# Kernel tuning notes

Hardware: AMD Instinct MI355X
Metric: run time of the kernel (lower is better)

## Reference

```python
import jax, jax.numpy as jnp
import numpy as np


def _linear_params(key, fan_in, fan_out):
    # torch nn.Linear default init: U(-1/sqrt(fan_in), 1/sqrt(fan_in))
    kw, kb = jax.random.split(key)
    bound = 1.0 / np.sqrt(fan_in)
    W = jax.random.uniform(kw, (fan_out, fan_in), jnp.float32, -bound, bound)
    b = jax.random.uniform(kb, (fan_out,), jnp.float32, -bound, bound)
    return W, b


def setup_inputs() -> dict:
    key = jax.random.key(0)
    kx, k1, k7, k8, k9 = jax.random.split(key, 5)
    x = jax.random.normal(kx, (4194304, 6), dtype=jnp.float32)
    W1, b1 = _linear_params(k1, 6, 8)
    W7, b7 = _linear_params(k7, 8, 4)
    W8, b8 = _linear_params(k8, 4, 2)
    W9, b9 = _linear_params(k9, 2, 1)
    return {"x": x, "W1": W1, "b1": b1, "W7": W7, "b7": b7,
            "W8": W8, "b8": b8, "W9": W9, "b9": b9}


def reference(x, W1, b1, W7, b7, W8, b8, W9, b9):
    # forward only uses l1 -> relu -> l7 -> relu -> l8 -> relu -> l9 -> softplus
    z = jax.nn.relu(x @ W1.T + b1)      # [N, 8]
    z = jax.nn.relu(z @ W7.T + b7)      # [N, 4]
    z = jax.nn.relu(z @ W8.T + b8)      # [N, 2]
    z = z @ W9.T + b9                   # [N, 1]
    return jax.nn.softplus(z)
```

## Files before the change

### kernel.cpp

```cpp
#include <hip/hip_runtime.h>
#include <math.h>


__device__ __forceinline__ float softplus_fast(float z) {
    float e = __expf(-fabsf(z));
    return fmaxf(z, 0.0f) + __logf(1.0f + e);
}

__global__ __launch_bounds__(256) void encoder_mlp_kernel(
    const float* __restrict__ x,
    const float* __restrict__ W1, const float* __restrict__ b1,
    const float* __restrict__ W7, const float* __restrict__ b7,
    const float* __restrict__ W8, const float* __restrict__ b8,
    const float* __restrict__ W9, const float* __restrict__ b9,
    float* __restrict__ out, int n_rows)
{
    const int t = blockIdx.x * blockDim.x + threadIdx.x;
    const long long row0 = (long long)t * 4;
    if (row0 >= n_rows) return;

    float xr[4][6];
    bool full_quad = (row0 + 4 <= n_rows);

    if (full_quad) {
        const float4* xin = reinterpret_cast<const float4*>(x) + (size_t)t * 6;
        float4 v0 = xin[0], v1 = xin[1], v2 = xin[2],
               v3 = xin[3], v4 = xin[4], v5 = xin[5];
        xr[0][0] = v0.x; xr[0][1] = v0.y; xr[0][2] = v0.z; xr[0][3] = v0.w; xr[0][4] = v1.x; xr[0][5] = v1.y;
        xr[1][0] = v1.z; xr[1][1] = v1.w; xr[1][2] = v2.x; xr[1][3] = v2.y; xr[1][4] = v2.z; xr[1][5] = v2.w;
        xr[2][0] = v3.x; xr[2][1] = v3.y; xr[2][2] = v3.z; xr[2][3] = v3.w; xr[2][4] = v4.x; xr[2][5] = v4.y;
        xr[3][0] = v4.z; xr[3][1] = v4.w; xr[3][2] = v5.x; xr[3][3] = v5.y; xr[3][4] = v5.z; xr[3][5] = v5.w;
    } else {
        #pragma unroll
        for (int r = 0; r < 4; ++r) {
            long long row = row0 + r;
            #pragma unroll
            for (int k = 0; k < 6; ++k)
                xr[r][k] = (row < n_rows) ? x[row * 6 + k] : 0.0f;
        }
    }

    float res[4];
    #pragma unroll
    for (int r = 0; r < 4; ++r) {
        float h1[8];
        #pragma unroll
        for (int j = 0; j < 8; ++j) {
            float acc = b1[j];
            #pragma unroll
            for (int k = 0; k < 6; ++k) acc = fmaf(W1[j * 6 + k], xr[r][k], acc);
            h1[j] = fmaxf(acc, 0.0f);
        }
        float h7[4];
        #pragma unroll
        for (int j = 0; j < 4; ++j) {
            float acc = b7[j];
            #pragma unroll
            for (int k = 0; k < 8; ++k) acc = fmaf(W7[j * 8 + k], h1[k], acc);
            h7[j] = fmaxf(acc, 0.0f);
        }
        float h8[2];
        #pragma unroll
        for (int j = 0; j < 2; ++j) {
            float acc = b8[j];
            #pragma unroll
            for (int k = 0; k < 4; ++k) acc = fmaf(W8[j * 4 + k], h7[k], acc);
            h8[j] = fmaxf(acc, 0.0f);
        }
        float z = fmaf(W9[0], h8[0], fmaf(W9[1], h8[1], b9[0]));
        res[r] = softplus_fast(z);
    }

    if (full_quad) {
        float4 o;
        o.x = res[0]; o.y = res[1]; o.z = res[2]; o.w = res[3];
        reinterpret_cast<float4*>(out)[t] = o;
    } else {
        #pragma unroll
        for (int r = 0; r < 4; ++r) {
            long long row = row0 + r;
            if (row < n_rows) out[row] = res[r];
        }
    }
}

extern "C" void kernel_launch(void* const* d_in, const int* in_sizes, int n_in,
                              void* d_out, int out_size, void* d_ws, size_t ws_size,
                              hipStream_t stream) {
    const float* x  = (const float*)d_in[0];
    const float* W1 = (const float*)d_in[1];
    const float* b1 = (const float*)d_in[2];
    const float* W7 = (const float*)d_in[3];
    const float* b7 = (const float*)d_in[4];
    const float* W8 = (const float*)d_in[5];
    const float* b8 = (const float*)d_in[6];
    const float* W9 = (const float*)d_in[7];
    const float* b9 = (const float*)d_in[8];
    float* out = (float*)d_out;

    const int n_rows = in_sizes[0] / 6;
    const int n_threads = (n_rows + 3) / 4;
    const int block = 256;
    const int grid = (n_threads + block - 1) / block;

    encoder_mlp_kernel<<<grid, block, 0, stream>>>(
        x, W1, b1, W7, b7, W8, b8, W9, b9, out, n_rows);
}
```

Before: 24.68 us.

## Process four quads per thread with double-buffered software-pipelined loads

Each thread now handles four row-quads strided by the grid size, loading the next quad into a second register buffer while computing the current one. The aim is more memory-level parallelism and load latency hidden behind the MLP arithmetic, with a quarter as many threads. The tail handling for row counts not divisible by four was dropped: partial quads are read and written as full float4 vectors, which can go out of bounds when n_rows is not a multiple of 4. It also raises register pressure.

```diff
diff --git a/kernel.cpp b/kernel.cpp
--- a/kernel.cpp
+++ b/kernel.cpp
@@ -1,46 +1,36 @@
 #include <hip/hip_runtime.h>
 #include <math.h>
 
+
+typedef float v4f __attribute__((ext_vector_type(4)));
 
 __device__ __forceinline__ float softplus_fast(float z) {
     float e = __expf(-fabsf(z));
     return fmaxf(z, 0.0f) + __logf(1.0f + e);
 }
 
-__global__ __launch_bounds__(256) void encoder_mlp_kernel(
-    const float* __restrict__ x,
+__device__ __forceinline__ void load_quad(const v4f* __restrict__ xin,
+                                          size_t q, v4f b[6]) {
+    const v4f* p = xin + q * 6;
+    b[0] = p[0]; b[1] = p[1]; b[2] = p[2];
+    b[3] = p[3]; b[4] = p[4]; b[5] = p[5];
+}
+
+__device__ __forceinline__ v4f compute_quad(
+    const v4f b[6],
     const float* __restrict__ W1, const float* __restrict__ b1,
     const float* __restrict__ W7, const float* __restrict__ b7,
     const float* __restrict__ W8, const float* __restrict__ b8,
-    const float* __restrict__ W9, const float* __restrict__ b9,
-    float* __restrict__ out, int n_rows)
+    const float* __restrict__ W9, const float* __restrict__ b9)
 {
-    const int t = blockIdx.x * blockDim.x + threadIdx.x;
-    const long long row0 = (long long)t * 4;
-    if (row0 >= n_rows) return;
+    float xr[4][6];
+    xr[0][0]=b[0].x; xr[0][1]=b[0].y; xr[0][2]=b[0].z; xr[0][3]=b[0].w; xr[0][4]=b[1].x; xr[0][5]=b[1].y;
+    xr[1][0]=b[1].z; xr[1][1]=b[1].w; xr[1][2]=b[2].x; xr[1][3]=b[2].y; xr[1][4]=b[2].z; xr[1][5]=b[2].w;
+    xr[2][0]=b[3].x; xr[2][1]=b[3].y; xr[2][2]=b[3].z; xr[2][3]=b[3].w; xr[2][4]=b[4].x; xr[2][5]=b[4].y;
+    xr[3][0]=b[4].z; xr[3][1]=b[4].w; xr[3][2]=b[5].x; xr[3][3]=b[5].y; xr[3][4]=b[5].z; xr[3][5]=b[5].w;
 
-    float xr[4][6];
-    bool full_quad = (row0 + 4 <= n_rows);
-
-    if (full_quad) {
-        const float4* xin = reinterpret_cast<const float4*>(x) + (size_t)t * 6;
-        float4 v0 = xin[0], v1 = xin[1], v2 = xin[2],
-               v3 = xin[3], v4 = xin[4], v5 = xin[5];
-        xr[0][0] = v0.x; xr[0][1] = v0.y; xr[0][2] = v0.z; xr[0][3] = v0.w; xr[0][4] = v1.x; xr[0][5] = v1.y;
-        xr[1][0] = v1.z; xr[1][1] = v1.w; xr[1][2] = v2.x; xr[1][3] = v2.y; xr[1][4] = v2.z; xr[1][5] = v2.w;
-        xr[2][0] = v3.x; xr[2][1] = v3.y; xr[2][2] = v3.z; xr[2][3] = v3.w; xr[2][4] = v4.x; xr[2][5] = v4.y;
-        xr[3][0] = v4.z; xr[3][1] = v4.w; xr[3][2] = v5.x; xr[3][3] = v5.y; xr[3][4] = v5.z; xr[3][5] = v5.w;
-    } else {
-        #pragma unroll
-        for (int r = 0; r < 4; ++r) {
-            long long row = row0 + r;
-            #pragma unroll
-            for (int k = 0; k < 6; ++k)
-                xr[r][k] = (row < n_rows) ? x[row * 6 + k] : 0.0f;
-        }
-    }
-
-    float res[4];
+    v4f res;
+    float out4[4];
     #pragma unroll
     for (int r = 0; r < 4; ++r) {
         float h1[8];
@@ -68,20 +58,48 @@
             h8[j] = fmaxf(acc, 0.0f);
         }
         float z = fmaf(W9[0], h8[0], fmaf(W9[1], h8[1], b9[0]));
-        res[r] = softplus_fast(z);
+        out4[r] = softplus_fast(z);
     }
+    res.x = out4[0]; res.y = out4[1]; res.z = out4[2]; res.w = out4[3];
+    return res;
+}
 
-    if (full_quad) {
-        float4 o;
-        o.x = res[0]; o.y = res[1]; o.z = res[2]; o.w = res[3];
-        reinterpret_cast<float4*>(out)[t] = o;
-    } else {
-        #pragma unroll
-        for (int r = 0; r < 4; ++r) {
-            long long row = row0 + r;
-            if (row < n_rows) out[row] = res[r];
-        }
-    }
+__global__ __launch_bounds__(256) void encoder_mlp_kernel(
+    const float* __restrict__ x,
+    const float* __restrict__ W1, const float* __restrict__ b1,
+    const float* __restrict__ W7, const float* __restrict__ b7,
+    const float* __restrict__ W8, const float* __restrict__ b8,
+    const float* __restrict__ W9, const float* __restrict__ b9,
+    float* __restrict__ out, int n_quads)
+{
+    const int t = blockIdx.x * blockDim.x + threadIdx.x;
+    const size_t nthreads = (size_t)gridDim.x * blockDim.x;
+    const v4f* xin = reinterpret_cast<const v4f*>(x);
+    v4f* outv = reinterpret_cast<v4f*>(out);
+
+    size_t q0 = (size_t)t;
+    size_t q1 = q0 + nthreads;
+    size_t q2 = q1 + nthreads;
+    size_t q3 = q2 + nthreads;
+
+    v4f bufA[6], bufB[6];
+
+    if (q0 < (size_t)n_quads) load_quad(xin, q0, bufA);
+    if (q1 < (size_t)n_quads) load_quad(xin, q1, bufB);
+
+    if (q0 < (size_t)n_quads)
+        outv[q0] = compute_quad(bufA, W1, b1, W7, b7, W8, b8, W9, b9);
+
+    if (q2 < (size_t)n_quads) load_quad(xin, q2, bufA);
+    if (q1 < (size_t)n_quads)
+        outv[q1] = compute_quad(bufB, W1, b1, W7, b7, W8, b8, W9, b9);
+
+    if (q3 < (size_t)n_quads) load_quad(xin, q3, bufB);
+    if (q2 < (size_t)n_quads)
+        outv[q2] = compute_quad(bufA, W1, b1, W7, b7, W8, b8, W9, b9);
+
+    if (q3 < (size_t)n_quads)
+        outv[q3] = compute_quad(bufB, W1, b1, W7, b7, W8, b8, W9, b9);
 }
 
 extern "C" void kernel_launch(void* const* d_in, const int* in_sizes, int n_in,
@@ -98,11 +116,14 @@
     const float* b9 = (const float*)d_in[8];
     float* out = (float*)d_out;
 
-    const int n_rows = in_sizes[0] / 6;
-    const int n_threads = (n_rows + 3) / 4;
+    const int n_rows  = in_sizes[0] / 6;
+    const int n_quads = (n_rows + 3) / 4;
+
     const int block = 256;
+    const int quads_per_thread = 4;
+    const int n_threads = (n_quads + quads_per_thread - 1) / quads_per_thread;
     const int grid = (n_threads + block - 1) / block;
 
     encoder_mlp_kernel<<<grid, block, 0, stream>>>(
-        x, W1, b1, W7, b7, W8, b8, W9, b9, out, n_rows);
+        x, W1, b1, W7, b7, W8, b8, W9, b9, out, n_quads);
 }
```

New measurement: 28.16 us. +14.1%, slower.
